# Optimization experiments

Measured on AMD Instinct MI355X. Metric: run time of the kernel, lower is better.

Reference implementation:

```python
import jax, jax.numpy as jnp
import numpy as np

B, S, DE, DR, H, V, R, L = 16, 128, 192, 64, 256, 100000, 64, 12
CAP = 20            # max tree depth enforced at generation time
NLEV = CAP + 1      # number of bottom-up levels (heights 0..CAP)


def setup_inputs() -> dict:
    rng = np.random.default_rng(0)
    # random dependency trees: node 0 is root, parent(i) in [0, i)
    heads = np.full((B, S), -1, np.int64)
    depth = np.zeros((B, S), np.int64)
    for b in range(B):
        for i in range(1, S):
            p = int(rng.integers(0, i))
            if depth[b, p] >= CAP:
                p = 0
            heads[b, i] = p
            depth[b, i] = depth[b, p] + 1
    # height = distance from deepest descendant leaf (leaves: 0)
    height = np.zeros((B, S), np.int64)
    for b in range(B):
        for i in range(S - 1, 0, -1):
            p = heads[b, i]
            if height[b, p] < height[b, i] + 1:
                height[b, p] = height[b, i] + 1
    base = (np.arange(B) * S)[:, None]
    child_idx = (base + np.arange(1, S)[None, :]).reshape(-1)   # [B*(S-1)]
    parent_idx = (base + heads[:, 1:]).reshape(-1)              # [B*(S-1)]

    key = jax.random.key(0)
    ks = jax.random.split(key, 16)
    u = lambda k, shape: jax.random.uniform(k, shape, jnp.float32, -0.08, 0.08)
    DIN = DE + DR
    return {
        "xs": jax.random.randint(ks[0], (B, S), 0, V),
        "rels": jax.random.randint(ks[1], (B, S), 0, R),
        "child_idx": jnp.asarray(child_idx),
        "parent_idx": jnp.asarray(parent_idx),
        "node_height": jnp.asarray(height.reshape(-1)),
        "n_levels": NLEV,
        "emb_W": u(ks[2], (V, DE)),
        "rel_W": u(ks[3], (R, DR)),
        "W_ix": u(ks[4], (DIN, H)), "b_ix": jnp.zeros((H,), jnp.float32),
        "W_ih": u(ks[5], (H, H)),   "b_ih": jnp.zeros((H,), jnp.float32),
        "W_fx": u(ks[6], (DIN, H)), "b_fx": jnp.zeros((H,), jnp.float32),
        "W_fh": u(ks[7], (H, H)),   "b_fh": jnp.zeros((H,), jnp.float32),
        "W_ox": u(ks[8], (DIN, H)), "W_oh": u(ks[9], (H, H)),
        "W_ux": u(ks[10], (DIN, H)), "W_uh": u(ks[11], (H, H)),
        "W_out": u(ks[12], (H, L)), "b_out": jnp.zeros((L,), jnp.float32),
    }


def reference(xs, rels, child_idx, parent_idx, node_height, n_levels,
              emb_W, rel_W, W_ix, b_ix, W_ih, b_ih, W_fx, b_fx, W_fh, b_fh,
              W_ox, W_oh, W_ux, W_uh, W_out, b_out):
    Bs, Ss = xs.shape
    N = Bs * Ss
    Hh = W_ih.shape[0]
    # embed + concat (dropout = identity in eval mode), flatten trees
    x = jnp.concatenate([emb_W[xs], rel_W[rels]], axis=-1).reshape(N, -1)  # [N, DIN]
    # input-side projections are level-invariant: hoist out of the recurrence
    ix = x @ W_ix + b_ix
    fx = x @ W_fx + b_fx
    ox = x @ W_ox
    ux = x @ W_ux

    h0 = jnp.zeros((N, Hh), x.dtype)
    c0 = jnp.zeros((N, Hh), x.dtype)

    def step(carry, level):
        h, c = carry
        h_ch = h[child_idx]                                   # [E, H]
        c_ch = c[child_idx]
        h_sum = jax.ops.segment_sum(h_ch, parent_idx, num_segments=N)
        # per-child forget gate (ChildSum); zero-padded children of the
        # original contribute f*0 = 0, so edges-only is exact
        f_e = jax.nn.sigmoid(h_ch @ W_fh + b_fh + fx[parent_idx])
        fc = jax.ops.segment_sum(f_e * c_ch, parent_idx, num_segments=N)
        i = jax.nn.sigmoid(ix + h_sum @ W_ih + b_ih)
        o = jax.nn.sigmoid(ox + h_sum @ W_oh)
        u_ = jnp.tanh(ux + h_sum @ W_uh)
        c_new = i * u_ + fc
        h_new = o * jnp.tanh(c_new)
        m = (node_height == level)[:, None]                   # commit this level only
        return (jnp.where(m, h_new, h), jnp.where(m, c_new, c)), None

    (h, _), _ = jax.lax.scan(step, (h0, c0), jnp.arange(n_levels))
    pooled = jnp.max(h.reshape(Bs, Ss, Hh), axis=1)           # max_pool1d over time
    return pooled @ W_out + b_out
```

## Files before the change

kernel.cpp:

```cpp
#include <hip/hip_runtime.h>
#include <hip/hip_bf16.h>

#define NN   2048
#define BB   16
#define SS   128
#define HH   256
#define DE   192
#define DR   64
#define DIN  256
#define LOUT 12
#define NLEV 21
#define TE   127

#define NT   16
#define CB   16
#define WC   16
#define RB   16
#define KP   264

#define SENT64 0xFFFFFFFFFFFFFFFFULL

typedef unsigned long long ull;
typedef __attribute__((ext_vector_type(8))) short short8v;
typedef __attribute__((ext_vector_type(4))) float f32x4;

__device__ __forceinline__ float sigm(float x){ return 1.f/(1.f + __expf(-x)); }

__device__ __forceinline__ short f2bf(float f){
    union { __hip_bfloat16 b; short s; } v; v.b = __float2bfloat16(f); return v.s;
}
__device__ __forceinline__ float bf2f(short s){
    union { unsigned u; float f; } v; v.u = ((unsigned)(unsigned short)s) << 16; return v.f;
}
__device__ __forceinline__ void st_dev(ull* p, ull v){
    __hip_atomic_store(p, v, __ATOMIC_RELAXED, __HIP_MEMORY_SCOPE_AGENT);
}
__device__ __forceinline__ ull ld_dev(const ull* p){
    return __hip_atomic_load(p, __ATOMIC_RELAXED, __HIP_MEMORY_SCOPE_AGENT);
}
__device__ __forceinline__ void st_devf(float* p, float v){
    __hip_atomic_store(p, v, __ATOMIC_RELAXED, __HIP_MEMORY_SCOPE_AGENT);
}
__device__ __forceinline__ int ld_devi(const int* p){
    return __hip_atomic_load(p, __ATOMIC_RELAXED, __HIP_MEMORY_SCOPE_AGENT);
}

__device__ __forceinline__ void barrier_lds(){
    __builtin_amdgcn_sched_barrier(0);
    asm volatile("s_waitcnt lgkmcnt(0)" ::: "memory");
    __builtin_amdgcn_s_barrier();
    __builtin_amdgcn_sched_barrier(0);
}

__device__ __forceinline__ void publish4(float hv, int cc, ull* rowp, int col0){
    unsigned p = (unsigned short)f2bf(hv);
    unsigned q = (unsigned)__shfl_xor((int)p, 1);
    unsigned pr = p | (q << 16);
    unsigned pr2 = (unsigned)__shfl_xor((int)pr, 2);
    if ((cc & 3) == 0)
        st_dev(rowp + ((col0 + cc) >> 2), pr | ((ull)pr2 << 32));
}

__global__ __launch_bounds__(256) void fill_k(ull* __restrict__ hx,
                                              int* __restrict__ pb)
{
    const int t = threadIdx.x;
    const size_t base = (size_t)blockIdx.x * 512 + t;
    st_dev(&hx[base], SENT64);
    st_dev(&hx[base + 256], SENT64);
    if (blockIdx.x == 0) {
        #pragma unroll
        for (int q = 0; q < (BB*HH)/256; ++q)
            __hip_atomic_store(&pb[q*256 + t], -1, __ATOMIC_RELAXED,
                               __HIP_MEMORY_SCOPE_AGENT);
    }
}

__global__ __launch_bounds__(256, 1) void tree_k(
    const int* __restrict__ xs, const int* __restrict__ rels,
    const float* __restrict__ emb_W, const float* __restrict__ rel_W,
    const float* __restrict__ W_ix, const float* __restrict__ b_ix,
    const float* __restrict__ W_fx, const float* __restrict__ b_fx,
    const float* __restrict__ W_ox, const float* __restrict__ W_ux,
    const int* __restrict__ child_idx, const int* __restrict__ parent_idx,
    const int* __restrict__ node_height,
    const float* __restrict__ W_ih, const float* __restrict__ b_ih,
    const float* __restrict__ W_fh, const float* __restrict__ b_fh,
    const float* __restrict__ W_oh, const float* __restrict__ W_uh,
    ull* __restrict__ hx, float* __restrict__ poolbuf,
    const float* __restrict__ W_out, const float* __restrict__ b_out,
    float* __restrict__ out)
{
    extern __shared__ __align__(16) char trans[];
    short* Wbf    = (short*)trans;
    short* hstage = (short*)(trans + 4*WC*KP*2);

    __shared__ float projL[4][SS][WC];
    __shared__ float cloc[SS][WC+1];
    __shared__ float hloc[SS][WC+1];
    __shared__ short hsrow[4][KP];
    __shared__ float biasF[WC], biasI[WC];
    __shared__ int loff[SS+1], lcur[SS], llist[SS];
    __shared__ int lvoff[NLEV+1], lvcur[NLEV], lvnodes[SS];
    __shared__ int s_maxH;

    const int t    = threadIdx.x;
    const int bid  = blockIdx.x;
    const int xcd  = bid & 7;
    const int idx  = bid >> 3;
    const int b    = xcd + 8 * (idx >> 4);
    const int cgp  = idx & 15;
    const int col0 = cgp * WC;
    const int cc   = t & 15;
    const int rr   = t >> 4;
    const int wv   = t >> 6;
    const int lane = t & 63;
    const int col  = lane & 15;
    const int kg   = lane >> 4;

    if (t < SS) { llist[t] = xs[b*SS + t]; lvnodes[t] = rels[b*SS + t]; lcur[t] = 0; }
    if (t < NLEV) lvcur[t] = 0;
    if (t == 0)   s_maxH = 0;
    __syncthreads();

    if (t < TE) { int p = parent_idx[b*TE + t] - b*SS; atomicAdd(&lcur[p], 1); }
    if (t < SS) { int hg = node_height[b*SS + t]; atomicAdd(&lvcur[hg], 1); atomicMax(&s_maxH, hg); }
    {
        const float* Wm4[4] = { W_fh, W_ih, W_oh, W_uh };
        for (int m = 0; m < 4; ++m) {
            short* dst = Wbf + (m*WC + cc)*KP;
            const float* src = Wm4[m] + col0 + cc;
            #pragma unroll 4
            for (int kb = 0; kb < 16; ++kb) {
                int k = kb*16 + rr;
                dst[k] = f2bf(src[(long long)k*HH]);
            }
        }
        if (t < WC) { biasF[t] = b_fh[col0+t]; biasI[t] = b_ih[col0+t]; }
    }
    short8v bfr[8];
    {
        const float* Wxm = (wv==0) ? W_ix : (wv==1) ? W_fx : (wv==2) ? W_ox : W_ux;
        #pragma unroll
        for (int f = 0; f < 8; ++f) {
            #pragma unroll
            for (int j = 0; j < 8; ++j)
                bfr[f][j] = f2bf(Wxm[(long long)(f*32 + kg*8 + j)*HH + col0 + col]);
        }
    }
    const float pbias = (wv==0) ? b_ix[col0+col] : (wv==1) ? b_fx[col0+col] : 0.f;

    short* xbf = hstage;
    for (int half = 0; half < 2; ++half) {
        __syncthreads();
        #pragma unroll
        for (int r2 = 0; r2 < 16; ++r2) {
            int gr = half*64 + wv*16 + r2;
            float4 v;
            if (lane < 48) v = *(const float4*)&emb_W[(long long)llist[gr]*DE + lane*4];
            else           v = *(const float4*)&rel_W[(long long)lvnodes[gr]*DR + (lane-48)*4];
            union { short s[4]; ull u; } pk;
            pk.s[0] = f2bf(v.x); pk.s[1] = f2bf(v.y);
            pk.s[2] = f2bf(v.z); pk.s[3] = f2bf(v.w);
            *(ull*)&xbf[(wv*16 + r2)*KP + lane*4] = pk.u;
        }
        __syncthreads();
        for (int lch = 0; lch < 4; ++lch) {
            f32x4 acc = {0.f,0.f,0.f,0.f};
            const short* ap = xbf + (lch*16 + col)*KP + kg*8;
            #pragma unroll
            for (int f = 0; f < 8; ++f)
                acc = __builtin_amdgcn_mfma_f32_16x16x32_bf16(
                    *(const short8v*)(ap + f*32), bfr[f], acc, 0,0,0);
            #pragma unroll
            for (int r = 0; r < 4; ++r)
                projL[wv][half*64 + lch*16 + kg*4 + r][col] = acc[r] + pbias;
        }
    }
    __syncthreads();

    short8v wfrF[8], wfrI[8], wfrO[8], wfrU[8];
    #pragma unroll
    for (int f = 0; f < 8; ++f) {
        const int o = col*KP + f*32 + kg*8;
        wfrF[f] = *(const short8v*)(Wbf + (0*WC)*KP + o);
        wfrI[f] = *(const short8v*)(Wbf + (1*WC)*KP + o);
        wfrO[f] = *(const short8v*)(Wbf + (2*WC)*KP + o);
        wfrU[f] = *(const short8v*)(Wbf + (3*WC)*KP + o);
    }

    if (t == 0) {
        int off = 0;
        for (int i = 0; i < SS; ++i) { int v = lcur[i]; loff[i] = off; lcur[i] = off; off += v; }
        loff[SS] = off;
        off = 0;
        for (int l2 = 0; l2 < NLEV; ++l2) { int v = lvcur[l2]; lvoff[l2] = off; lvcur[l2] = off; off += v; }
        lvoff[NLEV] = off;
    }
    __syncthreads();
    if (t < TE) {
        int e = b*TE + t;
        int p = parent_idx[e] - b*SS;
        int pos = atomicAdd(&lcur[p], 1);
        llist[pos] = child_idx[e] - b*SS;
    }
    if (t < SS) {
        int hg = node_height[b*SS + t];
        int pos = atomicAdd(&lvcur[hg], 1);
        lvnodes[pos] = t;
    }
    __syncthreads();

    short* Hst = hstage + wv*16*KP;
    const int mH = s_maxH;
    for (int lev = 0; lev <= mH; ++lev) {
        const int s0 = lvoff[lev], s1 = lvoff[lev+1];

        if (lev == 0) {
            for (int it = 0; s0 + it*16 + wv*4 < s1; ++it) {
                int j2 = s0 + it*16 + wv*4 + kg;
                if (j2 < s1) {
                    int n = lvnodes[j2];
                    float iv = sigm(projL[0][n][col] + biasI[col]);
                    float ov = sigm(projL[2][n][col]);
                    float uv = tanhf(projL[3][n][col]);
                    float cv = iv * uv;
                    float hv = ov * tanhf(cv);
                    cloc[n][col] = cv; hloc[n][col] = hv;
                    publish4(hv, col, hx + (size_t)(b*SS + n)*64, col0);
                }
            }
        } else {
            int j = s0 + wv;
            ull u[16]; int chr[4];
            int nOff = 0, nE = 0;
            if (j < s1) {
                int n0 = lvnodes[j]; nOff = loff[n0]; nE = loff[n0+1] - nOff;
                int m0 = min(nE, 16);
                #pragma unroll
                for (int rw = 0; rw < 4; ++rw) {
                    int e = kg + rw*4;
                    chr[rw] = (e < m0) ? llist[nOff + e] : -1;
                    if (chr[rw] >= 0) {
                        const ull* sp = hx + (size_t)(b*SS + chr[rw])*64 + col*4;
                        #pragma unroll
                        for (int q = 0; q < 4; ++q) u[rw*4+q] = ld_dev(sp+q);
                    }
                }
            }
            while (j < s1) {
                const int n = lvnodes[j];
                const int off = nOff, E = nE;
                float hs0=0.f, hs1=0.f, hs2=0.f, hs3=0.f, fpart=0.f;
                for (int fr = 0; fr < E; fr += 16) {
                    const int m = min(16, E - fr);
                    if (fr > 0) {
                        #pragma unroll
                        for (int rw = 0; rw < 4; ++rw) {
                            int e = kg + rw*4;
                            chr[rw] = (e < m) ? llist[off + fr + e] : -1;
                            if (chr[rw] >= 0) {
                                const ull* sp = hx + (size_t)(b*SS + chr[rw])*64 + col*4;
                                #pragma unroll
                                for (int q = 0; q < 4; ++q) u[rw*4+q] = ld_dev(sp+q);
                            }
                        }
                    }
                    for (;;) {
                        bool bad = false;
                        #pragma unroll
                        for (int rw = 0; rw < 4; ++rw)
                            if (chr[rw] >= 0) {
                                #pragma unroll
                                for (int q = 0; q < 4; ++q)
                                    bad = bad || (u[rw*4+q] == SENT64);
                            }
                        if (!bad) break;
                        __builtin_amdgcn_s_sleep(1);
                        #pragma unroll
                        for (int rw = 0; rw < 4; ++rw)
                            if (chr[rw] >= 0) {
                                const ull* sp = hx + (size_t)(b*SS + chr[rw])*64 + col*4;
                                #pragma unroll
                                for (int q = 0; q < 4; ++q)
                                    if (u[rw*4+q] == SENT64) u[rw*4+q] = ld_dev(sp+q);
                            }
                    }
                    #pragma unroll
                    for (int rw = 0; rw < 4; ++rw)
                        if (chr[rw] >= 0) {
                            int e = kg + rw*4;
                            ull* dp = (ull*)&Hst[e*KP + col*16];
                            dp[0]=u[rw*4]; dp[1]=u[rw*4+1]; dp[2]=u[rw*4+2]; dp[3]=u[rw*4+3];
                        }
                    f32x4 fa = {0.f,0.f,0.f,0.f};
                    {
                        const int ro = col*KP + kg*8;
                        #pragma unroll
                        for (int f = 0; f < 8; ++f)
                            fa = __builtin_amdgcn_mfma_f32_16x16x32_bf16(
                                *(const short8v*)(Hst + ro + f*32), wfrF[f], fa, 0,0,0);
                    }
                    #pragma unroll
                    for (int r = 0; r < 4; ++r) {
                        int e = kg*4 + r;
                        if (e < m) {
                            int ch2 = llist[off + fr + e];
                            float fg = sigm(fa[r] + biasF[col] + projL[1][n][col]);
                            fpart += fg * cloc[ch2][col];
                        }
                    }
                    for (int e = 0; e < m; ++e) {
                        union { short s[4]; ull v; } rv;
                        rv.v = *(const ull*)&Hst[e*KP + lane*4];
                        hs0 += bf2f(rv.s[0]); hs1 += bf2f(rv.s[1]);
                        hs2 += bf2f(rv.s[2]); hs3 += bf2f(rv.s[3]);
                    }
                }
                int jn = j + 4;
                if (jn < s1) {
                    int n1 = lvnodes[jn]; nOff = loff[n1]; nE = loff[n1+1] - nOff;
                    int m1 = min(nE, 16);
                    #pragma unroll
                    for (int rw = 0; rw < 4; ++rw) {
                        int e = kg + rw*4;
                        chr[rw] = (e < m1) ? llist[nOff + e] : -1;
                        if (chr[rw] >= 0) {
                            const ull* sp = hx + (size_t)(b*SS + chr[rw])*64 + col*4;
                            #pragma unroll
                            for (int q = 0; q < 4; ++q) u[rw*4+q] = ld_dev(sp+q);
                        }
                    }
                }
                {
                    union { short s[4]; ull v; } hp;
                    hp.s[0]=f2bf(hs0); hp.s[1]=f2bf(hs1);
                    hp.s[2]=f2bf(hs2); hp.s[3]=f2bf(hs3);
                    *(ull*)&hsrow[wv][lane*4] = hp.v;
                }
                f32x4 ia={0.f,0.f,0.f,0.f}, oa={0.f,0.f,0.f,0.f}, ua={0.f,0.f,0.f,0.f};
                {
                    const short* H = &hsrow[wv][0];
                    #pragma unroll
                    for (int f = 0; f < 8; ++f) {
                        short8v af = *(const short8v*)(H + f*32 + kg*8);
                        ia = __builtin_amdgcn_mfma_f32_16x16x32_bf16(af, wfrI[f], ia, 0,0,0);
                        oa = __builtin_amdgcn_mfma_f32_16x16x32_bf16(af, wfrO[f], oa, 0,0,0);
                        ua = __builtin_amdgcn_mfma_f32_16x16x32_bf16(af, wfrU[f], ua, 0,0,0);
                    }
                }
                fpart += __shfl_xor(fpart, 16);
                fpart += __shfl_xor(fpart, 32);
                if (lane < 16) {
                    float iv = sigm(projL[0][n][lane] + ia[0] + biasI[lane]);
                    float ov = sigm(projL[2][n][lane] + oa[0]);
                    float uv = tanhf(projL[3][n][lane] + ua[0]);
                    float cv = iv*uv + fpart;
                    float hv = ov * tanhf(cv);
                    cloc[n][lane] = cv; hloc[n][lane] = hv;
                    publish4(hv, lane, hx + (size_t)(b*SS + n)*64, col0);
                }
                j = jn;
            }
        }
        barrier_lds();
    }

    {
        float* pp = (float*)hstage;
        float mx = -3.4e38f;
        for (int s2 = rr; s2 < SS; s2 += RB)
            mx = fmaxf(mx, hloc[s2][cc]);
        pp[rr*17 + cc] = mx;
        __syncthreads();
        if (t < WC) {
            float m2 = pp[0*17 + t];
            #pragma unroll
            for (int r2 = 1; r2 < RB; ++r2) m2 = fmaxf(m2, pp[r2*17 + t]);
            st_devf(&poolbuf[b*HH + col0 + t], m2);
        }
    }
    if (cgp == 0) {
        const int* pb = (const int*)poolbuf + b*HH + t;
        int w = ld_devi(pb);
        while (w == -1) { __builtin_amdgcn_s_sleep(1); w = ld_devi(pb); }
        float* pl = (float*)&hsrow[0][0];
        pl[t] = __int_as_float(w);
        __syncthreads();
        if (t < LOUT) {
            float acc = b_out[t];
            for (int k = 0; k < HH; ++k)
                acc += pl[k] * W_out[k*LOUT + t];
            out[b*LOUT + t] = acc;
        }
    }
}

extern "C" void kernel_launch(void* const* d_in, const int* in_sizes, int n_in,
                              void* d_out, int out_size, void* d_ws, size_t ws_size,
                              hipStream_t stream)
{
    const int* xs          = (const int*)d_in[0];
    const int* rels        = (const int*)d_in[1];
    const int* child_idx   = (const int*)d_in[2];
    const int* parent_idx  = (const int*)d_in[3];
    const int* node_height = (const int*)d_in[4];
    const float* emb_W = (const float*)d_in[6];
    const float* rel_W = (const float*)d_in[7];
    const float* W_ix  = (const float*)d_in[8];
    const float* b_ix  = (const float*)d_in[9];
    const float* W_ih  = (const float*)d_in[10];
    const float* b_ih  = (const float*)d_in[11];
    const float* W_fx  = (const float*)d_in[12];
    const float* b_fx  = (const float*)d_in[13];
    const float* W_fh  = (const float*)d_in[14];
    const float* b_fh  = (const float*)d_in[15];
    const float* W_ox  = (const float*)d_in[16];
    const float* W_oh  = (const float*)d_in[17];
    const float* W_ux  = (const float*)d_in[18];
    const float* W_uh  = (const float*)d_in[19];
    const float* W_out = (const float*)d_in[20];
    const float* b_out = (const float*)d_in[21];

    ull*   hx      = (ull*)d_ws;
    float* poolbuf = (float*)((char*)d_ws + (size_t)NN*64*8);

    fill_k<<<256, 256, 0, stream>>>(hx, (int*)poolbuf);

    const unsigned int shmem = (unsigned int)(8u * WC * KP * 2);
    tree_k<<<dim3(NT*CB), dim3(256), shmem, stream>>>(
        xs, rels, emb_W, rel_W,
        W_ix, b_ix, W_fx, b_fx, W_ox, W_ux,
        child_idx, parent_idx, node_height,
        W_ih, b_ih, W_fh, b_fh, W_oh, W_uh,
        hx, poolbuf,
        W_out, b_out, (float*)d_out);
}
```

Measured before the change: 229.7 us.

## Replace per-level block barriers with dataflow scheduling over height-sorted nodes

Drops the level loop and its per-level workgroup barrier. Each wave now walks the height-sorted node list in strides of four and relies on the existing sentinel spin-wait on published child h values to enforce dependencies. Leaves now go through the same per-node path with zero children instead of a wide all-lane leaf pass. An lgkmcnt wait before publishing is meant to make the cell state in LDS visible before the global flag. The aim is to remove barrier stalls and load imbalance between levels, at the cost of less parallel leaf processing and reliance on cross-wave LDS ordering through a global flag.

```diff
diff --git a/kernel.cpp b/kernel.cpp
--- a/kernel.cpp
+++ b/kernel.cpp
@@ -43,13 +43,6 @@
 }
 __device__ __forceinline__ int ld_devi(const int* p){
     return __hip_atomic_load(p, __ATOMIC_RELAXED, __HIP_MEMORY_SCOPE_AGENT);
-}
-
-__device__ __forceinline__ void barrier_lds(){
-    __builtin_amdgcn_sched_barrier(0);
-    asm volatile("s_waitcnt lgkmcnt(0)" ::: "memory");
-    __builtin_amdgcn_s_barrier();
-    __builtin_amdgcn_sched_barrier(0);
 }
 
 __device__ __forceinline__ void publish4(float hv, int cc, ull* rowp, int col0){
@@ -212,46 +205,30 @@
     __syncthreads();
 
     short* Hst = hstage + wv*16*KP;
-    const int mH = s_maxH;
-    for (int lev = 0; lev <= mH; ++lev) {
-        const int s0 = lvoff[lev], s1 = lvoff[lev+1];
-
-        if (lev == 0) {
-            for (int it = 0; s0 + it*16 + wv*4 < s1; ++it) {
-                int j2 = s0 + it*16 + wv*4 + kg;
-                if (j2 < s1) {
-                    int n = lvnodes[j2];
-                    float iv = sigm(projL[0][n][col] + biasI[col]);
-                    float ov = sigm(projL[2][n][col]);
-                    float uv = tanhf(projL[3][n][col]);
-                    float cv = iv * uv;
-                    float hv = ov * tanhf(cv);
-                    cloc[n][col] = cv; hloc[n][col] = hv;
-                    publish4(hv, col, hx + (size_t)(b*SS + n)*64, col0);
+    {
+        int j = wv;
+        ull u[16]; int chr[4];
+        int nOff = 0, nE = 0;
+        {
+            int n0 = lvnodes[j]; nOff = loff[n0]; nE = loff[n0+1] - nOff;
+            int m0 = min(nE, 16);
+            #pragma unroll
+            for (int rw = 0; rw < 4; ++rw) {
+                int e = kg + rw*4;
+                chr[rw] = (e < m0) ? llist[nOff + e] : -1;
+                if (chr[rw] >= 0) {
+                    const ull* sp = hx + (size_t)(b*SS + chr[rw])*64 + col*4;
+                    #pragma unroll
+                    for (int q = 0; q < 4; ++q) u[rw*4+q] = ld_dev(sp+q);
                 }
             }
-        } else {
-            int j = s0 + wv;
-            ull u[16]; int chr[4];
-            int nOff = 0, nE = 0;
-            if (j < s1) {
-                int n0 = lvnodes[j]; nOff = loff[n0]; nE = loff[n0+1] - nOff;
-                int m0 = min(nE, 16);
-                #pragma unroll
-                for (int rw = 0; rw < 4; ++rw) {
-                    int e = kg + rw*4;
-                    chr[rw] = (e < m0) ? llist[nOff + e] : -1;
-                    if (chr[rw] >= 0) {
-                        const ull* sp = hx + (size_t)(b*SS + chr[rw])*64 + col*4;
-                        #pragma unroll
-                        for (int q = 0; q < 4; ++q) u[rw*4+q] = ld_dev(sp+q);
-                    }
-                }
-            }
-            while (j < s1) {
-                const int n = lvnodes[j];
-                const int off = nOff, E = nE;
-                float hs0=0.f, hs1=0.f, hs2=0.f, hs3=0.f, fpart=0.f;
+        }
+        while (j < SS) {
+            const int n = lvnodes[j];
+            const int off = nOff, E = nE;
+            float hs0=0.f, hs1=0.f, hs2=0.f, hs3=0.f, fpart=0.f;
+
+            if (E > 0) {
                 for (int fr = 0; fr < E; fr += 16) {
                     const int m = min(16, E - fr);
                     if (fr > 0) {
@@ -317,21 +294,26 @@
                         hs2 += bf2f(rv.s[2]); hs3 += bf2f(rv.s[3]);
                     }
                 }
-                int jn = j + 4;
-                if (jn < s1) {
-                    int n1 = lvnodes[jn]; nOff = loff[n1]; nE = loff[n1+1] - nOff;
-                    int m1 = min(nE, 16);
-                    #pragma unroll
-                    for (int rw = 0; rw < 4; ++rw) {
-                        int e = kg + rw*4;
-                        chr[rw] = (e < m1) ? llist[nOff + e] : -1;
-                        if (chr[rw] >= 0) {
-                            const ull* sp = hx + (size_t)(b*SS + chr[rw])*64 + col*4;
-                            #pragma unroll
-                            for (int q = 0; q < 4; ++q) u[rw*4+q] = ld_dev(sp+q);
-                        }
+            }
+
+            int jn = j + 4;
+            if (jn < SS) {
+                int n1 = lvnodes[jn]; nOff = loff[n1]; nE = loff[n1+1] - nOff;
+                int m1 = min(nE, 16);
+                #pragma unroll
+                for (int rw = 0; rw < 4; ++rw) {
+                    int e = kg + rw*4;
+                    chr[rw] = (e < m1) ? llist[nOff + e] : -1;
+                    if (chr[rw] >= 0) {
+                        const ull* sp = hx + (size_t)(b*SS + chr[rw])*64 + col*4;
+                        #pragma unroll
+                        for (int q = 0; q < 4; ++q) u[rw*4+q] = ld_dev(sp+q);
                     }
                 }
+            }
+
+            float dI = 0.f, dO = 0.f, dU = 0.f;
+            if (E > 0) {
                 {
                     union { short s[4]; ull v; } hp;
                     hp.s[0]=f2bf(hs0); hp.s[1]=f2bf(hs1);
@@ -349,22 +331,29 @@
                         ua = __builtin_amdgcn_mfma_f32_16x16x32_bf16(af, wfrU[f], ua, 0,0,0);
                     }
                 }
+                dI = ia[0]; dO = oa[0]; dU = ua[0];
                 fpart += __shfl_xor(fpart, 16);
                 fpart += __shfl_xor(fpart, 32);
-                if (lane < 16) {
-                    float iv = sigm(projL[0][n][lane] + ia[0] + biasI[lane]);
-                    float ov = sigm(projL[2][n][lane] + oa[0]);
-                    float uv = tanhf(projL[3][n][lane] + ua[0]);
-                    float cv = iv*uv + fpart;
-                    float hv = ov * tanhf(cv);
-                    cloc[n][lane] = cv; hloc[n][lane] = hv;
-                    publish4(hv, lane, hx + (size_t)(b*SS + n)*64, col0);
-                }
-                j = jn;
-            }
-        }
-        barrier_lds();
-    }
+            }
+
+            float hv = 0.f;
+            if (lane < 16) {
+                float iv = sigm(projL[0][n][lane] + dI + biasI[lane]);
+                float ov = sigm(projL[2][n][lane] + dO);
+                float uv = tanhf(projL[3][n][lane] + dU);
+                float cv = iv*uv + fpart;
+                hv = ov * tanhf(cv);
+                cloc[n][lane] = cv; hloc[n][lane] = hv;
+            }
+            __builtin_amdgcn_sched_barrier(0);
+            asm volatile("s_waitcnt lgkmcnt(0)" ::: "memory");
+            __builtin_amdgcn_sched_barrier(0);
+            if (lane < 16)
+                publish4(hv, lane, hx + (size_t)(b*SS + n)*64, col0);
+            j = jn;
+        }
+    }
+    __syncthreads();
 
     {
         float* pp = (float*)hstage;
```

New measurement: 243.5 us. +6.0%, slower.

## Double block size to eight waves and pipeline next-node child prefetch across levels

Applied to the files above, without the earlier changes.

Raises the tree kernel from 4 to 8 wavefronts per block, so twice as many tree nodes in a level are processed at once. The per-node child fragment shrinks from 16 to 8 children, and the staging LDS is resized to match. The prefetch of a wave's next node now carries across level barriers, so its loads can be issued before the barrier instead of after it. The cost is more register and LDS pressure per block, and nodes with many children need more fragment iterations.

```diff
diff --git a/kernel.cpp b/kernel.cpp
--- a/kernel.cpp
+++ b/kernel.cpp
@@ -15,7 +15,8 @@
 #define NT   16
 #define CB   16
 #define WC   16
-#define RB   16
+#define NW   8
+#define FR   8
 #define KP   264
 
 #define SENT64 0xFFFFFFFFFFFFFFFFULL
@@ -60,6 +61,22 @@
     if ((cc & 3) == 0)
         st_dev(rowp + ((col0 + cc) >> 2), pr | ((ull)pr2 << 32));
 }
+
+#define ISSUE_NODE(jj)                                                     \
+    if ((jj) < SS) {                                                       \
+        int n1_ = lvnodes[jj]; nOff = loff[n1_]; nE = loff[n1_+1] - nOff;  \
+        int m1_ = min(nE, FR);                                             \
+        _Pragma("unroll")                                                  \
+        for (int rw = 0; rw < 2; ++rw) {                                   \
+            int e_ = kg + rw*4;                                            \
+            chr[rw] = (e_ < m1_) ? llist[nOff + e_] : -1;                  \
+            if (chr[rw] >= 0) {                                            \
+                const ull* sp_ = hx + (size_t)(b*SS + chr[rw])*64 + col*4; \
+                _Pragma("unroll")                                          \
+                for (int q_ = 0; q_ < 4; ++q_) u[rw*4+q_] = ld_dev(sp_+q_);\
+            }                                                              \
+        }                                                                  \
+    }
 
 __global__ __launch_bounds__(256) void fill_k(ull* __restrict__ hx,
                                               int* __restrict__ pb)
@@ -76,7 +93,7 @@
     }
 }
 
-__global__ __launch_bounds__(256, 1) void tree_k(
+__global__ __launch_bounds__(512, 1) void tree_k(
     const int* __restrict__ xs, const int* __restrict__ rels,
     const float* __restrict__ emb_W, const float* __restrict__ rel_W,
     const float* __restrict__ W_ix, const float* __restrict__ b_ix,
@@ -98,7 +115,7 @@
     __shared__ float projL[4][SS][WC];
     __shared__ float cloc[SS][WC+1];
     __shared__ float hloc[SS][WC+1];
-    __shared__ short hsrow[4][KP];
+    __shared__ short hsrow[NW][KP];
     __shared__ float biasF[WC], biasI[WC];
     __shared__ int loff[SS+1], lcur[SS], llist[SS];
     __shared__ int lvoff[NLEV+1], lvcur[NLEV], lvnodes[SS];
@@ -112,11 +129,12 @@
     const int cgp  = idx & 15;
     const int col0 = cgp * WC;
     const int cc   = t & 15;
-    const int rr   = t >> 4;
     const int wv   = t >> 6;
     const int lane = t & 63;
     const int col  = lane & 15;
     const int kg   = lane >> 4;
+    const int gate = wv & 3;
+    const int ghalf= wv >> 2;
 
     if (t < SS) { llist[t] = xs[b*SS + t]; lvnodes[t] = rels[b*SS + t]; lcur[t] = 0; }
     if (t < NLEV) lvcur[t] = 0;
@@ -127,12 +145,14 @@
     if (t < SS) { int hg = node_height[b*SS + t]; atomicAdd(&lvcur[hg], 1); atomicMax(&s_maxH, hg); }
     {
         const float* Wm4[4] = { W_fh, W_ih, W_oh, W_uh };
-        for (int m = 0; m < 4; ++m) {
-            short* dst = Wbf + (m*WC + cc)*KP;
-            const float* src = Wm4[m] + col0 + cc;
+        const int ccw = t & 15, rrw = (t >> 4) & 15;
+        const int mm0 = (t >> 8) * 2;
+        for (int m = mm0; m < mm0 + 2; ++m) {
+            short* dst = Wbf + (m*WC + ccw)*KP;
+            const float* src = Wm4[m] + col0 + ccw;
             #pragma unroll 4
             for (int kb = 0; kb < 16; ++kb) {
-                int k = kb*16 + rr;
+                int k = kb*16 + rrw;
                 dst[k] = f2bf(src[(long long)k*HH]);
             }
         }
@@ -140,7 +160,7 @@
     }
     short8v bfr[8];
     {
-        const float* Wxm = (wv==0) ? W_ix : (wv==1) ? W_fx : (wv==2) ? W_ox : W_ux;
+        const float* Wxm = (gate==0) ? W_ix : (gate==1) ? W_fx : (gate==2) ? W_ox : W_ux;
         #pragma unroll
         for (int f = 0; f < 8; ++f) {
             #pragma unroll
@@ -148,33 +168,35 @@
                 bfr[f][j] = f2bf(Wxm[(long long)(f*32 + kg*8 + j)*HH + col0 + col]);
         }
     }
-    const float pbias = (wv==0) ? b_ix[col0+col] : (wv==1) ? b_fx[col0+col] : 0.f;
+    const float pbias = (gate==0) ? b_ix[col0+col] : (gate==1) ? b_fx[col0+col] : 0.f;
 
     short* xbf = hstage;
     for (int half = 0; half < 2; ++half) {
         __syncthreads();
         #pragma unroll
-        for (int r2 = 0; r2 < 16; ++r2) {
-            int gr = half*64 + wv*16 + r2;
+        for (int r2 = 0; r2 < 8; ++r2) {
+            int gr = half*64 + wv*8 + r2;
             float4 v;
             if (lane < 48) v = *(const float4*)&emb_W[(long long)llist[gr]*DE + lane*4];
             else           v = *(const float4*)&rel_W[(long long)lvnodes[gr]*DR + (lane-48)*4];
             union { short s[4]; ull u; } pk;
             pk.s[0] = f2bf(v.x); pk.s[1] = f2bf(v.y);
             pk.s[2] = f2bf(v.z); pk.s[3] = f2bf(v.w);
-            *(ull*)&xbf[(wv*16 + r2)*KP + lane*4] = pk.u;
+            *(ull*)&xbf[(wv*8 + r2)*KP + lane*4] = pk.u;
         }
         __syncthreads();
-        for (int lch = 0; lch < 4; ++lch) {
+        #pragma unroll
+        for (int lt = 0; lt < 2; ++lt) {
+            int tile = ghalf*2 + lt;
             f32x4 acc = {0.f,0.f,0.f,0.f};
-            const short* ap = xbf + (lch*16 + col)*KP + kg*8;
+            const short* ap = xbf + (tile*16 + col)*KP + kg*8;
             #pragma unroll
             for (int f = 0; f < 8; ++f)
                 acc = __builtin_amdgcn_mfma_f32_16x16x32_bf16(
                     *(const short8v*)(ap + f*32), bfr[f], acc, 0,0,0);
             #pragma unroll
             for (int r = 0; r < 4; ++r)
-                projL[wv][half*64 + lch*16 + kg*4 + r][col] = acc[r] + pbias;
+                projL[gate][half*64 + tile*16 + kg*4 + r][col] = acc[r] + pbias;
         }
     }
     __syncthreads();
@@ -211,52 +233,44 @@
     }
     __syncthreads();
 
-    short* Hst = hstage + wv*16*KP;
     const int mH = s_maxH;
-    for (int lev = 0; lev <= mH; ++lev) {
-        const int s0 = lvoff[lev], s1 = lvoff[lev+1];
-
-        if (lev == 0) {
-            for (int it = 0; s0 + it*16 + wv*4 < s1; ++it) {
-                int j2 = s0 + it*16 + wv*4 + kg;
-                if (j2 < s1) {
-                    int n = lvnodes[j2];
-                    float iv = sigm(projL[0][n][col] + biasI[col]);
-                    float ov = sigm(projL[2][n][col]);
-                    float uv = tanhf(projL[3][n][col]);
-                    float cv = iv * uv;
-                    float hv = ov * tanhf(cv);
-                    cloc[n][col] = cv; hloc[n][col] = hv;
-                    publish4(hv, col, hx + (size_t)(b*SS + n)*64, col0);
-                }
+    {
+        const int s0 = lvoff[0], s1 = lvoff[1];
+        for (int it = 0; s0 + it*(NW*4) + wv*4 < s1; ++it) {
+            int j2 = s0 + it*(NW*4) + wv*4 + kg;
+            if (j2 < s1) {
+                int n = lvnodes[j2];
+                float iv = sigm(projL[0][n][col] + biasI[col]);
+                float ov = sigm(projL[2][n][col]);
+                float uv = tanhf(projL[3][n][col]);
+                float cv = iv * uv;
+                float hv = ov * tanhf(cv);
+                cloc[n][col] = cv; hloc[n][col] = hv;
+                publish4(hv, col, hx + (size_t)(b*SS + n)*64, col0);
             }
-        } else {
-            int j = s0 + wv;
-            ull u[16]; int chr[4];
-            int nOff = 0, nE = 0;
-            if (j < s1) {
-                int n0 = lvnodes[j]; nOff = loff[n0]; nE = loff[n0+1] - nOff;
-                int m0 = min(nE, 16);
-                #pragma unroll
-                for (int rw = 0; rw < 4; ++rw) {
-                    int e = kg + rw*4;
-                    chr[rw] = (e < m0) ? llist[nOff + e] : -1;
-                    if (chr[rw] >= 0) {
-                        const ull* sp = hx + (size_t)(b*SS + chr[rw])*64 + col*4;
-                        #pragma unroll
-                        for (int q = 0; q < 4; ++q) u[rw*4+q] = ld_dev(sp+q);
-                    }
-                }
-            }
+        }
+    }
+
+    short* Hst = hstage + wv*FR*KP;
+    {
+        int j = lvoff[1] + wv;
+        ull u[8]; int chr[2];
+        int nOff = 0, nE = 0;
+        ISSUE_NODE(j);
+        barrier_lds();
+
+        for (int lev = 1; lev <= mH; ++lev) {
+            const int s1 = lvoff[lev+1];
             while (j < s1) {
                 const int n = lvnodes[j];
                 const int off = nOff, E = nE;
                 float hs0=0.f, hs1=0.f, hs2=0.f, hs3=0.f, fpart=0.f;
-                for (int fr = 0; fr < E; fr += 16) {
-                    const int m = min(16, E - fr);
+
+                for (int fr = 0; fr < E; fr += FR) {
+                    const int m = min(FR, E - fr);
                     if (fr > 0) {
                         #pragma unroll
-                        for (int rw = 0; rw < 4; ++rw) {
+                        for (int rw = 0; rw < 2; ++rw) {
                             int e = kg + rw*4;
                             chr[rw] = (e < m) ? llist[off + fr + e] : -1;
                             if (chr[rw] >= 0) {
@@ -269,7 +283,7 @@
                     for (;;) {
                         bool bad = false;
                         #pragma unroll
-                        for (int rw = 0; rw < 4; ++rw)
+                        for (int rw = 0; rw < 2; ++rw)
                             if (chr[rw] >= 0) {
                                 #pragma unroll
                                 for (int q = 0; q < 4; ++q)
@@ -278,7 +292,7 @@
                         if (!bad) break;
                         __builtin_amdgcn_s_sleep(1);
                         #pragma unroll
-                        for (int rw = 0; rw < 4; ++rw)
+                        for (int rw = 0; rw < 2; ++rw)
                             if (chr[rw] >= 0) {
                                 const ull* sp = hx + (size_t)(b*SS + chr[rw])*64 + col*4;
                                 #pragma unroll
@@ -287,7 +301,7 @@
                             }
                     }
                     #pragma unroll
-                    for (int rw = 0; rw < 4; ++rw)
+                    for (int rw = 0; rw < 2; ++rw)
                         if (chr[rw] >= 0) {
                             int e = kg + rw*4;
                             ull* dp = (ull*)&Hst[e*KP + col*16];
@@ -295,7 +309,7 @@
                         }
                     f32x4 fa = {0.f,0.f,0.f,0.f};
                     {
-                        const int ro = col*KP + kg*8;
+                        const int ro = (col & 7)*KP + kg*8;
                         #pragma unroll
                         for (int f = 0; f < 8; ++f)
                             fa = __builtin_amdgcn_mfma_f32_16x16x32_bf16(
@@ -317,21 +331,10 @@
                         hs2 += bf2f(rv.s[2]); hs3 += bf2f(rv.s[3]);
                     }
                 }
-                int jn = j + 4;
-                if (jn < s1) {
-                    int n1 = lvnodes[jn]; nOff = loff[n1]; nE = loff[n1+1] - nOff;
-                    int m1 = min(nE, 16);
-                    #pragma unroll
-                    for (int rw = 0; rw < 4; ++rw) {
-                        int e = kg + rw*4;
-                        chr[rw] = (e < m1) ? llist[nOff + e] : -1;
-                        if (chr[rw] >= 0) {
-                            const ull* sp = hx + (size_t)(b*SS + chr[rw])*64 + col*4;
-                            #pragma unroll
-                            for (int q = 0; q < 4; ++q) u[rw*4+q] = ld_dev(sp+q);
-                        }
-                    }
-                }
+
+                int jn = j + NW;
+                ISSUE_NODE(jn);
+
                 {
                     union { short s[4]; ull v; } hp;
                     hp.s[0]=f2bf(hs0); hp.s[1]=f2bf(hs1);
@@ -362,30 +365,33 @@
                 }
                 j = jn;
             }
-        }
-        barrier_lds();
+            barrier_lds();
+        }
     }
 
     {
         float* pp = (float*)hstage;
+        const int rp = t >> 4;
         float mx = -3.4e38f;
-        for (int s2 = rr; s2 < SS; s2 += RB)
+        for (int s2 = rp; s2 < SS; s2 += 32)
             mx = fmaxf(mx, hloc[s2][cc]);
-        pp[rr*17 + cc] = mx;
+        pp[rp*17 + cc] = mx;
         __syncthreads();
         if (t < WC) {
             float m2 = pp[0*17 + t];
             #pragma unroll
-            for (int r2 = 1; r2 < RB; ++r2) m2 = fmaxf(m2, pp[r2*17 + t]);
+            for (int r2 = 1; r2 < 32; ++r2) m2 = fmaxf(m2, pp[r2*17 + t]);
             st_devf(&poolbuf[b*HH + col0 + t], m2);
         }
     }
     if (cgp == 0) {
-        const int* pb = (const int*)poolbuf + b*HH + t;
-        int w = ld_devi(pb);
-        while (w == -1) { __builtin_amdgcn_s_sleep(1); w = ld_devi(pb); }
         float* pl = (float*)&hsrow[0][0];
-        pl[t] = __int_as_float(w);
+        if (t < HH) {
+            const int* pb = (const int*)poolbuf + b*HH + t;
+            int w = ld_devi(pb);
+            while (w == -1) { __builtin_amdgcn_s_sleep(1); w = ld_devi(pb); }
+            pl[t] = __int_as_float(w);
+        }
         __syncthreads();
         if (t < LOUT) {
             float acc = b_out[t];
@@ -427,8 +433,8 @@
 
     fill_k<<<256, 256, 0, stream>>>(hx, (int*)poolbuf);
 
-    const unsigned int shmem = (unsigned int)(8u * WC * KP * 2);
-    tree_k<<<dim3(NT*CB), dim3(256), shmem, stream>>>(
+    const unsigned int shmem = (unsigned int)((4*WC + NW*FR) * KP * 2);
+    tree_k<<<dim3(NT*CB), dim3(512), shmem, stream>>>(
         xs, rels, emb_W, rel_W,
         W_ix, b_ix, W_fx, b_fx, W_ox, W_ux,
         child_idx, parent_idx, node_height,
```

New measurement: 205.4 us. 10.6% less time.
